# Performance work log

Measured on AMD Instinct MI355X. Metric: run time of the kernel, lower is better.

## Reference

```python
import jax, jax.numpy as jnp
import numpy as np

DT = 1.0
EPS = 1e-6


def setup_inputs() -> dict:
    key = jax.random.key(0)
    ks = jax.random.split(key, 5)
    B, I, H = 8192, 512, 1024
    scale = (6.0 / ((1 + 5.0) * (I + H))) ** 0.5  # kaiming_uniform with a=sqrt(5) bound
    return {
        "x": jax.random.normal(ks[0], (B, I), dtype=jnp.float32),
        "hidden": jax.random.normal(ks[1], (B, H), dtype=jnp.float32),
        "W_tau": jax.random.uniform(ks[2], (H, I + H), dtype=jnp.float32, minval=-scale, maxval=scale),
        "b_tau": jnp.zeros((H,), dtype=jnp.float32),
        "W_r": jax.random.uniform(ks[3], (H, I + H), dtype=jnp.float32, minval=-scale, maxval=scale),
        "b_r": jnp.zeros((H,), dtype=jnp.float32),
        "W_h": jax.random.uniform(ks[4], (H, I + H), dtype=jnp.float32, minval=-scale, maxval=scale),
        "b_h": jnp.zeros((H,), dtype=jnp.float32),
    }


def reference(x, hidden, W_tau, b_tau, W_r, b_r, W_h, b_h):
    combined = jnp.concatenate([x, hidden], axis=1)          # [B, I+H]
    tau = jax.nn.softplus(combined @ W_tau.T + b_tau) + EPS  # [B, H]
    r = jax.nn.sigmoid(combined @ W_r.T + b_r)               # [B, H]
    gated = r * hidden
    cand_in = jnp.concatenate([x, gated], axis=1)            # [B, I+H]
    h_tilde = jnp.tanh(cand_in @ W_h.T + b_h)                # [B, H]
    return hidden + DT * (h_tilde - hidden) / tau
```

## Files before the change

kernel.cpp:

```cpp
#include <hip/hip_runtime.h>
#include <hip/hip_bf16.h>

typedef __attribute__((ext_vector_type(8))) unsigned short u16x8;
typedef __attribute__((ext_vector_type(8))) __bf16        bf16x8;
typedef __attribute__((ext_vector_type(4))) float         f32x4;

static constexpr int B_ = 8192;
static constexpr int I_ = 512;
static constexpr int H_ = 1024;
static constexpr int K_ = 1536;
static constexpr int NT = K_ / 64;

#define AS1 __attribute__((address_space(1)))
#define AS3 __attribute__((address_space(3)))

__device__ __forceinline__ unsigned short f2bf(float f) {
    unsigned int u = __float_as_uint(f);
    u += 0x7FFF + ((u >> 16) & 1);
    return (unsigned short)(u >> 16);
}
__device__ __forceinline__ float bf2f(unsigned short u) {
    return __uint_as_float(((unsigned int)u) << 16);
}

__device__ __forceinline__ void memfence() { asm volatile("" ::: "memory"); }
__device__ __forceinline__ void barrier_() {
    memfence(); __builtin_amdgcn_s_barrier(); memfence();
}
__device__ __forceinline__ void vwait6() {
    asm volatile("s_waitcnt vmcnt(6)" ::: "memory");
    __builtin_amdgcn_sched_barrier(0);
}
__device__ __forceinline__ void vwait12() {
    asm volatile("s_waitcnt vmcnt(12)" ::: "memory");
    __builtin_amdgcn_sched_barrier(0);
}
__device__ __forceinline__ void lgkmfence() {
    asm volatile("s_waitcnt lgkmcnt(15)" ::: "memory");
    __builtin_amdgcn_sched_barrier(0);
}

__device__ __forceinline__ u16x8 cvt8(const float4* s) {
    float4 a = s[0], b = s[1];
    u16x8 o;
    o[0] = f2bf(a.x); o[1] = f2bf(a.y); o[2] = f2bf(a.z); o[3] = f2bf(a.w);
    o[4] = f2bf(b.x); o[5] = f2bf(b.y); o[6] = f2bf(b.z); o[7] = f2bf(b.w);
    return o;
}

__global__ void prep(const float* __restrict__ x, const float* __restrict__ hid,
                     const float* __restrict__ wt, const float* __restrict__ wr,
                     const float* __restrict__ wh,
                     unsigned short* __restrict__ cmb1,
                     unsigned short* __restrict__ wtb,
                     unsigned short* __restrict__ wrb,
                     unsigned short* __restrict__ whb) {
    constexpr int NX8 = B_ * I_ / 8;
    constexpr int NH8 = B_ * H_ / 8;
    constexpr int NW8 = H_ * K_ / 8;
    int i = blockIdx.x * blockDim.x + threadIdx.x;
    if (i < NX8) {
        int row = i >> 6, c8 = i & 63;
        u16x8 o = cvt8((const float4*)x + (size_t)i * 2);
        *(u16x8*)(cmb1 + (size_t)row * K_ + c8 * 8) = o;
    } else if (i < NX8 + NH8) {
        int j = i - NX8;
        int row = j >> 7, c8 = j & 127;
        u16x8 o = cvt8((const float4*)hid + (size_t)j * 2);
        *(u16x8*)(cmb1 + (size_t)row * K_ + 512 + c8 * 8) = o;
    } else {
        int k = i - (NX8 + NH8);
        const float* src; unsigned short* dst;
        if (k < NW8)          { src = wt; dst = wtb; }
        else if (k < 2 * NW8) { src = wr; dst = wrb; k -= NW8; }
        else                  { src = wh; dst = whb; k -= 2 * NW8; }
        u16x8 o = cvt8((const float4*)src + (size_t)k * 2);
        *(u16x8*)(dst + (size_t)k * 8) = o;
    }
}

template<int MODE>
__global__ __launch_bounds__(512, 1)
void gemmP(const unsigned short* __restrict__ A1,
           const unsigned short* __restrict__ A2,
           const unsigned short* __restrict__ W,
           const float* __restrict__ bias,
           const unsigned short* __restrict__ itau_in,
           float* __restrict__ outF,
           unsigned short* __restrict__ itau_out,
           unsigned short* __restrict__ gate_out)
{
    extern __shared__ __align__(16) char lds[];

    const int t = threadIdx.x;
    const int w = t >> 6, l = t & 63;
    const int wg  = blockIdx.y * 8 + blockIdx.x;
    const int swz = (wg & 7) * 32 + (wg >> 3);
    const int m0  = (swz >> 3) * 256;
    const int n0  = (swz & 7) * 128;

    const int srow  = t >> 3;
    const int sslot = ((t & 7) ^ (srow & 7)) * 8;
    const unsigned short* srcA1 = A1 + (size_t)(m0 + srow) * K_ + sslot;
    const unsigned short* srcA2 = A2 + (size_t)(m0 + srow) * K_ + sslot;
    const unsigned short* srcB  = W  + (size_t)(n0 + srow) * K_ + sslot;

    auto stageTile = [&](int bi, int ts) {
        const unsigned short* sA = ((MODE == 2 && ts >= 8) ? srcA2 : srcA1) + ts * 64;
        char* dA = lds + bi * 32768 + w * 1024;
        #pragma unroll
        for (int q = 0; q < 4; ++q)
            __builtin_amdgcn_global_load_lds(
                (const AS1 void*)(sA + (size_t)q * 64 * K_),
                (AS3 void*)(dA + q * 8192), 16, 0, 0);
        const unsigned short* sB = srcB + ts * 64;
        char* dB = lds + 98304 + bi * 16384 + w * 1024;
        #pragma unroll
        for (int h = 0; h < 2; ++h)
            __builtin_amdgcn_global_load_lds(
                (const AS1 void*)(sB + (size_t)(h * 64) * K_),
                (AS3 void*)(dB + h * 8192), 16, 0, 0);
    };

    const int fr = l & 15, kq = l >> 4;
    const int wm = w >> 1, wn = w & 1;
    const int fx = (kq ^ (fr & 7)) << 4;
    const char* rdA0 = lds + (wm * 32 + fr) * 128 + fx;
    const char* rdA1 = lds + (wm * 32 + fr) * 128 + (fx ^ 64);
    const char* rdB0 = lds + 98304 + (wn * 32 + fr) * 128 + fx;
    const char* rdB1 = lds + 98304 + (wn * 32 + fr) * 128 + (fx ^ 64);

    struct Frags { bf16x8 a[4][2]; bf16x8 b[4][2]; };
    Frags fE, fO;
    f32x4 acc[4][4];
    #pragma unroll
    for (int i = 0; i < 4; ++i)
        #pragma unroll
        for (int jn = 0; jn < 4; ++jn) acc[i][jn] = (f32x4)0.0f;

    auto readTile = [&](Frags& f, int bi) {
        #pragma unroll
        for (int mf = 0; mf < 4; ++mf) {
            const int off = bi * 32768 + (mf >> 1) * 16384 + (mf & 1) * 2048;
            f.a[mf][0] = *(const bf16x8*)(rdA0 + off);
            f.a[mf][1] = *(const bf16x8*)(rdA1 + off);
        }
        #pragma unroll
        for (int nf = 0; nf < 4; ++nf) {
            const int off = bi * 16384 + (nf >> 1) * 8192 + (nf & 1) * 2048;
            f.b[nf][0] = *(const bf16x8*)(rdB0 + off);
            f.b[nf][1] = *(const bf16x8*)(rdB1 + off);
        }
    };
    auto mfma64 = [&](const Frags& f) {
        __builtin_amdgcn_s_setprio(1);
        #pragma unroll
        for (int mf = 0; mf < 4; ++mf)
            #pragma unroll
            for (int nf = 0; nf < 4; ++nf)
                #pragma unroll
                for (int ks = 0; ks < 2; ++ks)
                    acc[mf][nf] = __builtin_amdgcn_mfma_f32_16x16x32_bf16(
                        f.a[mf][ks], f.b[nf][ks], acc[mf][nf], 0, 0, 0);
        __builtin_amdgcn_s_setprio(0);
    };

    stageTile(0, 0); stageTile(1, 1); stageTile(2, 2);
    vwait12(); barrier_();
    readTile(fE, 0);

    #define CLMP(X) (((X) < NT) ? (X) : 0)
    for (int j = 0; j < 4; ++j) {
        const int t0 = 6 * j;
        vwait6(); barrier_();
        readTile(fO, 1); lgkmfence(); stageTile(0, CLMP(t0 + 3)); mfma64(fE);
        vwait6(); barrier_();
        readTile(fE, 2); lgkmfence(); stageTile(1, CLMP(t0 + 4)); mfma64(fO);
        vwait6(); barrier_();
        readTile(fO, 0); lgkmfence(); stageTile(2, CLMP(t0 + 5)); mfma64(fE);
        vwait6(); barrier_();
        readTile(fE, 1); lgkmfence(); stageTile(0, CLMP(t0 + 6)); mfma64(fO);
        vwait6(); barrier_();
        readTile(fO, 2); lgkmfence(); stageTile(1, CLMP(t0 + 7)); mfma64(fE);
        vwait6(); barrier_();
        readTile(fE, 0); lgkmfence(); stageTile(2, CLMP(t0 + 8)); mfma64(fO);
    }
    #undef CLMP
    asm volatile("s_waitcnt vmcnt(0)" ::: "memory");

    const int rs4 = kq * 4;
    #pragma unroll
    for (int mf = 0; mf < 4; ++mf)
        #pragma unroll
        for (int nf = 0; nf < 4; ++nf) {
            const int n = n0 + (nf >> 1) * 64 + wn * 32 + (nf & 1) * 16 + fr;
            const float bv = bias[n];
            #pragma unroll
            for (int jj = 0; jj < 4; ++jj) {
                const int m = m0 + (mf >> 1) * 128 + wm * 32 + (mf & 1) * 16 + rs4 + jj;
                const size_t ix = (size_t)m * H_ + n;
                const size_t hx = (size_t)m * K_ + 512 + n;
                const float z = acc[mf][nf][jj] + bv;
                if (MODE == 0) {
                    const float sp = (z > 15.f) ? z : __logf(1.0f + __expf(z));
                    itau_out[ix] = f2bf(__fdividef(1.0f, sp + 1e-6f));
                } else if (MODE == 1) {
                    const float r = __fdividef(1.0f, 1.0f + __expf(-z));
                    gate_out[hx] = f2bf(r * bf2f(A1[hx]));
                } else {
                    const float e2 = __expf(2.0f * z);
                    const float th = __fdividef(e2 - 1.0f, e2 + 1.0f);
                    const float h = bf2f(A1[hx]);
                    const float it = bf2f(itau_in[ix]);
                    outF[ix] = h + (th - h) * it;
                }
            }
        }
}

extern "C" void kernel_launch(void* const* d_in, const int* in_sizes, int n_in,
                              void* d_out, int out_size, void* d_ws, size_t ws_size,
                              hipStream_t stream) {
    (void)in_sizes; (void)n_in; (void)out_size; (void)ws_size;

    const float* x     = (const float*)d_in[0];
    const float* hid   = (const float*)d_in[1];
    const float* W_tau = (const float*)d_in[2];
    const float* b_tau = (const float*)d_in[3];
    const float* W_r   = (const float*)d_in[4];
    const float* b_r   = (const float*)d_in[5];
    const float* W_h   = (const float*)d_in[6];
    const float* b_h   = (const float*)d_in[7];

    unsigned short* cmb1 = (unsigned short*)d_ws;
    unsigned short* cmb2 = cmb1 + (size_t)B_ * K_;
    unsigned short* wtb  = cmb2 + (size_t)B_ * K_;
    unsigned short* wrb  = wtb  + (size_t)H_ * K_;
    unsigned short* whb  = wrb  + (size_t)H_ * K_;
    unsigned short* itau = whb  + (size_t)H_ * K_;

    hipFuncSetAttribute(reinterpret_cast<const void*>(&gemmP<0>),
                        hipFuncAttributeMaxDynamicSharedMemorySize, 147456);
    hipFuncSetAttribute(reinterpret_cast<const void*>(&gemmP<1>),
                        hipFuncAttributeMaxDynamicSharedMemorySize, 147456);
    hipFuncSetAttribute(reinterpret_cast<const void*>(&gemmP<2>),
                        hipFuncAttributeMaxDynamicSharedMemorySize, 147456);

    const int th = 256;
    constexpr int NPREP = B_ * I_ / 8 + B_ * H_ / 8 + 3 * H_ * K_ / 8;
    prep<<<NPREP / th, th, 0, stream>>>(x, hid, W_tau, W_r, W_h,
                                        cmb1, wtb, wrb, whb);

    dim3 g(8, 32);
    gemmP<0><<<g, 512, 147456, stream>>>(cmb1, cmb1, wtb, b_tau, nullptr,
                                         nullptr, itau, nullptr);
    gemmP<1><<<g, 512, 147456, stream>>>(cmb1, cmb1, wrb, b_r, nullptr,
                                         nullptr, nullptr, cmb2);
    gemmP<2><<<g, 512, 147456, stream>>>(cmb1, cmb2, whb, b_h, itau,
                                         (float*)d_out, nullptr, nullptr);
}
```

Before: 111.3 us.

## Replace 256x128 triple-buffered GEMM with 128x128 double-buffered two-blocks-per-CU kernel

The three GEMM stages move from 512-thread blocks with 256x128 tiles and a three-stage LDS pipeline with fragment double-buffering to 256-thread blocks with 128x128 tiles and a simple two-buffer loop. LDS per block shrinks to 64 KB so two blocks can share a CU, which trades intra-block software pipelining for inter-block latency hiding. The new loop waits on all outstanding loads every iteration and halves data reuse per block, so global and L2 traffic goes up and the loads within a block overlap less.

```diff
diff --git a/kernel.cpp b/kernel.cpp
--- a/kernel.cpp
+++ b/kernel.cpp
@@ -27,16 +27,8 @@
 __device__ __forceinline__ void barrier_() {
     memfence(); __builtin_amdgcn_s_barrier(); memfence();
 }
-__device__ __forceinline__ void vwait6() {
-    asm volatile("s_waitcnt vmcnt(6)" ::: "memory");
-    __builtin_amdgcn_sched_barrier(0);
-}
-__device__ __forceinline__ void vwait12() {
-    asm volatile("s_waitcnt vmcnt(12)" ::: "memory");
-    __builtin_amdgcn_sched_barrier(0);
-}
-__device__ __forceinline__ void lgkmfence() {
-    asm volatile("s_waitcnt lgkmcnt(15)" ::: "memory");
+__device__ __forceinline__ void vwait0() {
+    asm volatile("s_waitcnt vmcnt(0)" ::: "memory");
     __builtin_amdgcn_sched_barrier(0);
 }
 
@@ -80,8 +72,8 @@
 }
 
 template<int MODE>
-__global__ __launch_bounds__(512, 1)
-void gemmP(const unsigned short* __restrict__ A1,
+__global__ __launch_bounds__(256, 2)
+void gemmT(const unsigned short* __restrict__ A1,
            const unsigned short* __restrict__ A2,
            const unsigned short* __restrict__ W,
            const float* __restrict__ bias,
@@ -95,8 +87,8 @@
     const int t = threadIdx.x;
     const int w = t >> 6, l = t & 63;
     const int wg  = blockIdx.y * 8 + blockIdx.x;
-    const int swz = (wg & 7) * 32 + (wg >> 3);
-    const int m0  = (swz >> 3) * 256;
+    const int swz = (wg & 7) * 64 + (wg >> 3);
+    const int m0  = (swz >> 3) * 128;
     const int n0  = (swz & 7) * 128;
 
     const int srow  = t >> 3;
@@ -107,52 +99,49 @@
 
     auto stageTile = [&](int bi, int ts) {
         const unsigned short* sA = ((MODE == 2 && ts >= 8) ? srcA2 : srcA1) + ts * 64;
-        char* dA = lds + bi * 32768 + w * 1024;
+        char* dA = lds + bi * 16384 + w * 1024;
         #pragma unroll
         for (int q = 0; q < 4; ++q)
             __builtin_amdgcn_global_load_lds(
-                (const AS1 void*)(sA + (size_t)q * 64 * K_),
-                (AS3 void*)(dA + q * 8192), 16, 0, 0);
+                (const AS1 void*)(sA + (size_t)q * 32 * K_),
+                (AS3 void*)(dA + q * 4096), 16, 0, 0);
         const unsigned short* sB = srcB + ts * 64;
-        char* dB = lds + 98304 + bi * 16384 + w * 1024;
-        #pragma unroll
-        for (int h = 0; h < 2; ++h)
+        char* dB = lds + 32768 + bi * 16384 + w * 1024;
+        #pragma unroll
+        for (int q = 0; q < 4; ++q)
             __builtin_amdgcn_global_load_lds(
-                (const AS1 void*)(sB + (size_t)(h * 64) * K_),
-                (AS3 void*)(dB + h * 8192), 16, 0, 0);
+                (const AS1 void*)(sB + (size_t)q * 32 * K_),
+                (AS3 void*)(dB + q * 4096), 16, 0, 0);
     };
 
     const int fr = l & 15, kq = l >> 4;
     const int wm = w >> 1, wn = w & 1;
     const int fx = (kq ^ (fr & 7)) << 4;
-    const char* rdA0 = lds + (wm * 32 + fr) * 128 + fx;
-    const char* rdA1 = lds + (wm * 32 + fr) * 128 + (fx ^ 64);
-    const char* rdB0 = lds + 98304 + (wn * 32 + fr) * 128 + fx;
-    const char* rdB1 = lds + 98304 + (wn * 32 + fr) * 128 + (fx ^ 64);
-
-    struct Frags { bf16x8 a[4][2]; bf16x8 b[4][2]; };
-    Frags fE, fO;
+    const char* rdA0 = lds + (wm * 64 + fr) * 128 + fx;
+    const char* rdA1 = lds + (wm * 64 + fr) * 128 + (fx ^ 64);
+    const char* rdB0 = lds + 32768 + (wn * 64 + fr) * 128 + fx;
+    const char* rdB1 = lds + 32768 + (wn * 64 + fr) * 128 + (fx ^ 64);
+
+    bf16x8 af[4][2], bfr[4][2];
     f32x4 acc[4][4];
     #pragma unroll
     for (int i = 0; i < 4; ++i)
         #pragma unroll
         for (int jn = 0; jn < 4; ++jn) acc[i][jn] = (f32x4)0.0f;
 
-    auto readTile = [&](Frags& f, int bi) {
+    auto readFrags = [&](int bi) {
         #pragma unroll
         for (int mf = 0; mf < 4; ++mf) {
-            const int off = bi * 32768 + (mf >> 1) * 16384 + (mf & 1) * 2048;
-            f.a[mf][0] = *(const bf16x8*)(rdA0 + off);
-            f.a[mf][1] = *(const bf16x8*)(rdA1 + off);
+            af[mf][0] = *(const bf16x8*)(rdA0 + bi * 16384 + mf * 2048);
+            af[mf][1] = *(const bf16x8*)(rdA1 + bi * 16384 + mf * 2048);
         }
         #pragma unroll
         for (int nf = 0; nf < 4; ++nf) {
-            const int off = bi * 16384 + (nf >> 1) * 8192 + (nf & 1) * 2048;
-            f.b[nf][0] = *(const bf16x8*)(rdB0 + off);
-            f.b[nf][1] = *(const bf16x8*)(rdB1 + off);
+            bfr[nf][0] = *(const bf16x8*)(rdB0 + bi * 16384 + nf * 2048);
+            bfr[nf][1] = *(const bf16x8*)(rdB1 + bi * 16384 + nf * 2048);
         }
     };
-    auto mfma64 = [&](const Frags& f) {
+    auto mfma32 = [&]() {
         __builtin_amdgcn_s_setprio(1);
         #pragma unroll
         for (int mf = 0; mf < 4; ++mf)
@@ -161,43 +150,31 @@
                 #pragma unroll
                 for (int ks = 0; ks < 2; ++ks)
                     acc[mf][nf] = __builtin_amdgcn_mfma_f32_16x16x32_bf16(
-                        f.a[mf][ks], f.b[nf][ks], acc[mf][nf], 0, 0, 0);
+                        af[mf][ks], bfr[nf][ks], acc[mf][nf], 0, 0, 0);
         __builtin_amdgcn_s_setprio(0);
     };
 
-    stageTile(0, 0); stageTile(1, 1); stageTile(2, 2);
-    vwait12(); barrier_();
-    readTile(fE, 0);
-
-    #define CLMP(X) (((X) < NT) ? (X) : 0)
-    for (int j = 0; j < 4; ++j) {
-        const int t0 = 6 * j;
-        vwait6(); barrier_();
-        readTile(fO, 1); lgkmfence(); stageTile(0, CLMP(t0 + 3)); mfma64(fE);
-        vwait6(); barrier_();
-        readTile(fE, 2); lgkmfence(); stageTile(1, CLMP(t0 + 4)); mfma64(fO);
-        vwait6(); barrier_();
-        readTile(fO, 0); lgkmfence(); stageTile(2, CLMP(t0 + 5)); mfma64(fE);
-        vwait6(); barrier_();
-        readTile(fE, 1); lgkmfence(); stageTile(0, CLMP(t0 + 6)); mfma64(fO);
-        vwait6(); barrier_();
-        readTile(fO, 2); lgkmfence(); stageTile(1, CLMP(t0 + 7)); mfma64(fE);
-        vwait6(); barrier_();
-        readTile(fE, 0); lgkmfence(); stageTile(2, CLMP(t0 + 8)); mfma64(fO);
+    stageTile(0, 0);
+    vwait0(); barrier_();
+
+    for (int ts = 0; ts < NT; ++ts) {
+        const int bi = ts & 1;
+        stageTile(bi ^ 1, (ts + 1 < NT) ? ts + 1 : 0);
+        readFrags(bi);
+        mfma32();
+        vwait0(); barrier_();
     }
-    #undef CLMP
-    asm volatile("s_waitcnt vmcnt(0)" ::: "memory");
 
     const int rs4 = kq * 4;
     #pragma unroll
     for (int mf = 0; mf < 4; ++mf)
         #pragma unroll
         for (int nf = 0; nf < 4; ++nf) {
-            const int n = n0 + (nf >> 1) * 64 + wn * 32 + (nf & 1) * 16 + fr;
+            const int n = n0 + wn * 64 + nf * 16 + fr;
             const float bv = bias[n];
             #pragma unroll
             for (int jj = 0; jj < 4; ++jj) {
-                const int m = m0 + (mf >> 1) * 128 + wm * 32 + (mf & 1) * 16 + rs4 + jj;
+                const int m = m0 + wm * 64 + mf * 16 + rs4 + jj;
                 const size_t ix = (size_t)m * H_ + n;
                 const size_t hx = (size_t)m * K_ + 512 + n;
                 const float z = acc[mf][nf][jj] + bv;
@@ -239,23 +216,23 @@
     unsigned short* whb  = wrb  + (size_t)H_ * K_;
     unsigned short* itau = whb  + (size_t)H_ * K_;
 
-    hipFuncSetAttribute(reinterpret_cast<const void*>(&gemmP<0>),
-                        hipFuncAttributeMaxDynamicSharedMemorySize, 147456);
-    hipFuncSetAttribute(reinterpret_cast<const void*>(&gemmP<1>),
-                        hipFuncAttributeMaxDynamicSharedMemorySize, 147456);
-    hipFuncSetAttribute(reinterpret_cast<const void*>(&gemmP<2>),
-                        hipFuncAttributeMaxDynamicSharedMemorySize, 147456);
+    hipFuncSetAttribute(reinterpret_cast<const void*>(&gemmT<0>),
+                        hipFuncAttributeMaxDynamicSharedMemorySize, 65536);
+    hipFuncSetAttribute(reinterpret_cast<const void*>(&gemmT<1>),
+                        hipFuncAttributeMaxDynamicSharedMemorySize, 65536);
+    hipFuncSetAttribute(reinterpret_cast<const void*>(&gemmT<2>),
+                        hipFuncAttributeMaxDynamicSharedMemorySize, 65536);
 
     const int th = 256;
     constexpr int NPREP = B_ * I_ / 8 + B_ * H_ / 8 + 3 * H_ * K_ / 8;
     prep<<<NPREP / th, th, 0, stream>>>(x, hid, W_tau, W_r, W_h,
                                         cmb1, wtb, wrb, whb);
 
-    dim3 g(8, 32);
-    gemmP<0><<<g, 512, 147456, stream>>>(cmb1, cmb1, wtb, b_tau, nullptr,
-                                         nullptr, itau, nullptr);
-    gemmP<1><<<g, 512, 147456, stream>>>(cmb1, cmb1, wrb, b_r, nullptr,
-                                         nullptr, nullptr, cmb2);
-    gemmP<2><<<g, 512, 147456, stream>>>(cmb1, cmb2, whb, b_h, itau,
-                                         (float*)d_out, nullptr, nullptr);
-}
+    dim3 g(8, 64);
+    gemmT<0><<<g, 256, 65536, stream>>>(cmb1, cmb1, wtb, b_tau, nullptr,
+                                        nullptr, itau, nullptr);
+    gemmT<1><<<g, 256, 65536, stream>>>(cmb1, cmb1, wrb, b_r, nullptr,
+                                        nullptr, nullptr, cmb2);
+    gemmT<2><<<g, 256, 65536, stream>>>(cmb1, cmb2, whb, b_h, itau,
+                                        (float*)d_out, nullptr, nullptr);
+}
```

Measured after the change: 110.9 us. About the same (-0.4%).
